# Kernel tuning notes

Hardware: AMD Instinct MI355X
Metric: run time of the kernel (lower is better)

The kernel has to match this reference:

```python
import jax, jax.numpy as jnp
import numpy as np

D_MODEL = 1024
H = 16
D_K = D_MODEL // H
B, S = 2, 2048


def setup_inputs() -> dict:
    key = jax.random.key(0)
    ks = jax.random.split(key, 11)
    sc = 1.0 / np.sqrt(D_MODEL)
    inp = {
        "q": jax.random.normal(ks[0], (B, S, D_MODEL), jnp.float32),
        "k": jax.random.normal(ks[1], (B, S, D_MODEL), jnp.float32),
        "v": jax.random.normal(ks[2], (B, S, D_MODEL), jnp.float32),
        "mask": jnp.ones((1, 1, S, S), dtype=bool),
        # nn.Linear weights are [out, in]; y = x @ W.T + b
        "wq_w": jax.random.normal(ks[3], (D_MODEL, D_MODEL), jnp.float32) * sc,
        "wq_b": jnp.zeros((D_MODEL,), jnp.float32),
        "wk_w": jax.random.normal(ks[4], (D_MODEL, D_MODEL), jnp.float32) * sc,
        "wk_b": jnp.zeros((D_MODEL,), jnp.float32),
        "wv_w": jax.random.normal(ks[5], (D_MODEL, D_MODEL), jnp.float32) * sc,
        "wv_b": jnp.zeros((D_MODEL,), jnp.float32),
        "wo_w": jax.random.normal(ks[6], (D_MODEL, D_MODEL), jnp.float32) * sc,
        "wo_b": jnp.zeros((D_MODEL,), jnp.float32),
    }
    return inp


def _split_heads(x):
    b, s, _ = x.shape
    return x.reshape(b, s, H, D_K).transpose(0, 2, 1, 3)  # [B,H,S,Dk]


def reference(q, k, v, mask, wq_w, wq_b, wk_w, wk_b, wv_w, wv_b, wo_w, wo_b):
    # projections (nn.Linear: x @ W.T + b)
    qh = _split_heads(q @ wq_w.T + wq_b)
    kh = _split_heads(k @ wk_w.T + wk_b)
    vh = _split_heads(v @ wv_w.T + wv_b)
    # scaled dot-product attention with additive -1e9 masking
    scores = jnp.einsum("bhqd,bhkd->bhqk", qh, kh) / jnp.sqrt(jnp.float32(D_K))
    scores = jnp.where(mask, scores, jnp.float32(-1e9))
    attn = jax.nn.softmax(scores, axis=-1)  # dropout p=0.0 -> identity
    out = jnp.einsum("bhqk,bhkd->bhqd", attn, vh)
    out = out.transpose(0, 2, 1, 3).reshape(q.shape[0], q.shape[1], D_MODEL)
    return out @ wo_w.T + wo_b
```

## Files before the change

kernel.cpp:

```cpp
#include <hip/hip_runtime.h>
#include <hip/hip_bf16.h>


typedef unsigned short u16;
typedef unsigned int u32;
typedef short s16x4 __attribute__((ext_vector_type(4)));
typedef short s16x8 __attribute__((ext_vector_type(8)));
typedef float f32x4 __attribute__((ext_vector_type(4)));
typedef unsigned int u32x2 __attribute__((ext_vector_type(2)));
typedef unsigned int u32x4 __attribute__((ext_vector_type(4)));

#define NH 16
#define SCQ 0.1803368801111204f

__device__ __forceinline__ float bf2f(u16 h) {
  u32 u = ((u32)h) << 16;
  return __builtin_bit_cast(float, u);
}
__device__ __forceinline__ u16 f2bf(float f) {
  u32 u = __builtin_bit_cast(u32, f);
  u32 r = (u + 0x7fffu + ((u >> 16) & 1u)) >> 16;
  return (u16)r;
}

__device__ __forceinline__ u32 pk2(float a, float b) {
#if __has_builtin(__builtin_amdgcn_cvt_pk_bf16_f32)
  typedef __bf16 bf2_t __attribute__((ext_vector_type(2)));
  bf2_t r = __builtin_amdgcn_cvt_pk_bf16_f32(a, b);
  return __builtin_bit_cast(u32, r);
#else
  u32 ua = __builtin_bit_cast(u32, a) + 0x8000u;
  u32 ub = __builtin_bit_cast(u32, b) + 0x8000u;
  return __builtin_amdgcn_perm(ub, ua, 0x07060302);
#endif
}

__device__ __forceinline__ void stage16(const void* g, void* l) {
  __builtin_amdgcn_global_load_lds((const __attribute__((address_space(1))) void*)g,
                                   (__attribute__((address_space(3))) void*)l,
                                   16, 0, 0);
}

#define BAR() __builtin_amdgcn_s_barrier()
#define WAITV2 asm volatile("s_waitcnt vmcnt(2)" ::: "memory")
#define WAITV0 asm volatile("s_waitcnt vmcnt(0)" ::: "memory")

__global__ __launch_bounds__(256) void convert_all(
    const float* __restrict__ q, const float* __restrict__ k,
    const float* __restrict__ v, const float* __restrict__ wq,
    const float* __restrict__ wk, const float* __restrict__ wv,
    const float* __restrict__ wo, u16* qb, u16* kb, u16* vb, u16* wqb,
    u16* wkb, u16* wvb, u16* wob) {
  const int y = blockIdx.y;
  const float* s;
  u16* d;
  int i;
  if (y < 3) {
    s = y == 0 ? q : (y == 1 ? k : v);
    d = y == 0 ? qb : (y == 1 ? kb : vb);
    i = (blockIdx.x * 256 + threadIdx.x) * 4;
  } else {
    int w = blockIdx.x >> 10, j = blockIdx.x & 1023;
    s = w == 0 ? wq : (w == 1 ? wk : (w == 2 ? wv : wo));
    d = w == 0 ? wqb : (w == 1 ? wkb : (w == 2 ? wvb : wob));
    i = (j * 256 + threadIdx.x) * 4;
  }
  f32x4 val = *(const f32x4*)(s + i);
  u32x2 o = {pk2(val[0], val[1]), pk2(val[2], val[3])};
  *(u32x2*)(d + i) = o;
}

#define GEMM_CORE(A_, W_)                                                      \
  const int tid = threadIdx.x;                                                 \
  const int lane = tid & 63;                                                   \
  const int wid = tid >> 6;                                                    \
  const int l16 = lane & 15, quad = lane >> 4;                                 \
  const int wm = (wid >> 1) * 64, wn = (wid & 1) * 64;                         \
  const int m0 = blockIdx.y * 128;                                             \
  const int n0 = blockIdx.x * 128;                                             \
  const int ra = tid >> 2;                                                     \
  const int c8 = (tid & 3) ^ (ra & 3);                                         \
  const u16* Abase = A_ + (size_t)(m0 + ra) * 1024 + c8 * 8;                   \
  const u16* A2 = Abase + (size_t)64 * 1024;                                   \
  const u16* Wbase = W_ + (size_t)(n0 + ra) * 1024 + c8 * 8;                   \
  const u16* W2 = Wbase + (size_t)64 * 1024;                                   \
  u16* ldsA = As + tid * 8;                                                    \
  u16* ldsB = Bs + tid * 8;                                                    \
  f32x4 acc[4][4];                                                             \
  _Pragma("unroll") for (int i = 0; i < 4; ++i)                                \
  _Pragma("unroll") for (int j = 0; j < 4; ++j)                                \
      acc[i][j] = (f32x4){0.f, 0.f, 0.f, 0.f};                                 \
  for (int k0 = 0; k0 < 1024; k0 += 32) {                                      \
    __syncthreads();                                                           \
    stage16(Abase + k0, ldsA);                                                 \
    stage16(A2 + k0, ldsA + 2048);                                             \
    stage16(Wbase + k0, ldsB);                                                 \
    stage16(W2 + k0, ldsB + 2048);                                             \
    __syncthreads();                                                           \
    s16x8 bfr[4];                                                              \
    _Pragma("unroll") for (int j = 0; j < 4; ++j) {                            \
      int row = wn + j * 16 + l16;                                             \
      bfr[j] = *(const s16x8*)&Bs[(row * 4 + (quad ^ (row & 3))) * 8];         \
    }                                                                          \
    _Pragma("unroll") for (int i = 0; i < 4; ++i) {                            \
      int row = wm + i * 16 + l16;                                             \
      s16x8 afr = *(const s16x8*)&As[(row * 4 + (quad ^ (row & 3))) * 8];      \
      _Pragma("unroll") for (int j = 0; j < 4; ++j)                            \
        acc[i][j] =                                                            \
            __builtin_amdgcn_mfma_f32_16x16x32_bf16(afr, bfr[j], acc[i][j],    \
                                                    0, 0, 0);                  \
    }                                                                          \
  }

__global__ __launch_bounds__(256, 3) void proj_kernel(
    const u16* __restrict__ q, const u16* __restrict__ k, const u16* __restrict__ v,
    const u16* __restrict__ wq, const u16* __restrict__ wk, const u16* __restrict__ wv,
    const float* __restrict__ bq, const float* __restrict__ bk,
    const float* __restrict__ bv,
    u16* __restrict__ Qh, u16* __restrict__ Kh, u16* __restrict__ VhT) {
  const int z = blockIdx.z;
  const u16* A_in = z == 0 ? q : (z == 1 ? k : v);
  const u16* W_in = z == 0 ? wq : (z == 1 ? wk : wv);
  const float* bias = z == 0 ? bq : (z == 1 ? bk : bv);

  __shared__ __align__(16) u16 As[128 * 32];
  __shared__ __align__(16) u16 Bs[128 * 32];

  GEMM_CORE(A_in, W_in)

  float bcol[4];
#pragma unroll
  for (int j = 0; j < 4; ++j) bcol[j] = bias[n0 + wn + j * 16 + l16];

  if (z < 2) {
    const float qs = (z == 0) ? SCQ : 1.0f;
    u16* out = (z == 0) ? Qh : Kh;
#pragma unroll
    for (int i = 0; i < 4; ++i) {
      int gm0 = m0 + wm + i * 16 + quad * 4;
      int b = gm0 >> 11, s = gm0 & 2047;
#pragma unroll
      for (int j = 0; j < 4; ++j) {
        int gn = n0 + wn + j * 16 + l16;
        int h = gn >> 6, dk = gn & 63;
        size_t base = ((size_t)(b * NH + h) * 2048 + s) * 64 + dk;
#pragma unroll
        for (int r = 0; r < 4; ++r)
          out[base + (size_t)r * 64] = f2bf((acc[i][j][r] + bcol[j]) * qs);
      }
    }
  } else {
#pragma unroll
    for (int i = 0; i < 4; ++i) {
      int gm0 = m0 + wm + i * 16 + quad * 4;
      int b = gm0 >> 11, s = gm0 & 2047;
#pragma unroll
      for (int j = 0; j < 4; ++j) {
        int gn = n0 + wn + j * 16 + l16;
        int h = gn >> 6, dk = gn & 63;
        size_t base = ((size_t)(b * NH + h) * 64 + dk) * 2048 + s;
        u32x2 pv = {pk2(acc[i][j][0] + bcol[j], acc[i][j][1] + bcol[j]),
                    pk2(acc[i][j][2] + bcol[j], acc[i][j][3] + bcol[j])};
        *(u32x2*)&VhT[base] = pv;
      }
    }
  }
}

__global__ __launch_bounds__(256, 3) void out_kernel(const u16* __restrict__ ctx,
                                                     const u16* __restrict__ wo,
                                                     const float* __restrict__ bo,
                                                     float* __restrict__ out) {
  __shared__ __align__(16) u16 As[128 * 32];
  __shared__ __align__(16) u16 Bs[128 * 32];

  GEMM_CORE(ctx, wo)

  float bcol[4];
#pragma unroll
  for (int j = 0; j < 4; ++j) bcol[j] = bo[n0 + wn + j * 16 + l16];

#pragma unroll
  for (int i = 0; i < 4; ++i) {
    int gm0 = m0 + wm + i * 16 + quad * 4;
#pragma unroll
    for (int j = 0; j < 4; ++j) {
      int gn = n0 + wn + j * 16 + l16;
#pragma unroll
      for (int r = 0; r < 4; ++r)
        out[(size_t)(gm0 + r) * 1024 + gn] = acc[i][j][r] + bcol[j];
    }
  }
}

__global__ __launch_bounds__(512, 4) void flash_kernel(const u16* __restrict__ Qh,
                                                       const u16* __restrict__ Kh,
                                                       const u16* __restrict__ VhT,
                                                       u16* __restrict__ ctx) {
  __shared__ __align__(16) u16 smem[16384];

  const int tid = threadIdx.x;
  const int lane = tid & 63;
  const int wid = tid >> 6;
  const int l16 = lane & 15, quad = lane >> 4;
  const int qt = blockIdx.x;
  const int bh = blockIdx.y;

  const u16* Qg = Qh + ((size_t)bh * 2048 + qt * 256) * 64;
  const u16* Kg = Kh + (size_t)bh * 2048 * 64;
  const u16* Vg = VhT + (size_t)bh * 64 * 2048;

  const int rq = tid >> 3;
  const int c8 = (tid & 7) ^ (rq & 7);
  const int gq = ((rq & 15) >> 2) * 8 + (rq & 3) + (((rq >> 4) & 1) << 2);
  const int ksrc = (rq & 32) + gq;

#define ISSUE_TILE(KT)                                                        \
  {                                                                           \
    stage16(Kg + (size_t)((KT) * 64 + ksrc) * 64 + c8 * 8,                    \
            smem + ((KT) & 1) * 4096 + tid * 8);                              \
    stage16(Vg + (size_t)rq * 2048 + (KT) * 64 + c8 * 8,                      \
            smem + 8192 + ((KT) & 1) * 4096 + tid * 8);                       \
  }

  u16* Qs = smem;
  s16x8 bq[2][2];
  for (int p = 0; p < 2; ++p) {
#pragma unroll
    for (int i = 0; i < 2; ++i)
      stage16(Qg + (size_t)(p * 128 + rq + i * 64) * 64 + c8 * 8,
              Qs + tid * 8 + i * 4096);
    __syncthreads();
    if ((wid >> 2) == p) {
#pragma unroll
      for (int ct = 0; ct < 2; ++ct) {
        int row = (wid & 3) * 32 + ct * 16 + l16;
#pragma unroll
        for (int kk = 0; kk < 2; ++kk)
          bq[ct][kk] =
              *(const s16x8*)&Qs[(row * 8 + ((kk * 4 + quad) ^ (row & 7))) * 8];
      }
    }
    asm volatile("s_waitcnt lgkmcnt(0)" ::: "memory");
    __syncthreads();
  }

  const s16x8 a1 = {0x3F80, 0x3F80, 0x3F80, 0x3F80,
                    0x3F80, 0x3F80, 0x3F80, 0x3F80};

  f32x4 lf[2];
  f32x4 oacc[4][2];
#pragma unroll
  for (int ct = 0; ct < 2; ++ct) lf[ct] = (f32x4){0.f, 0.f, 0.f, 0.f};
#pragma unroll
  for (int d = 0; d < 4; ++d)
#pragma unroll
    for (int ct = 0; ct < 2; ++ct) oacc[d][ct] = (f32x4){0.f, 0.f, 0.f, 0.f};

  ISSUE_TILE(0);

  for (int kt = 0; kt < 32; ++kt) {
    const u16* Ks = smem + (kt & 1) * 4096;
    const u16* Vs = smem + 8192 + (kt & 1) * 4096;

    BAR();
    if (kt < 31) {
      ISSUE_TILE(kt + 1);
      WAITV2;
    } else {
      WAITV0;
    }
    BAR();

    f32x4 st[4][2];
    __builtin_amdgcn_s_setprio(1);
#pragma unroll
    for (int rt = 0; rt < 4; ++rt) {
      int row = rt * 16 + l16;
      s16x8 ak0 = *(const s16x8*)&Ks[(row * 8 + (quad ^ (row & 7))) * 8];
      s16x8 ak1 = *(const s16x8*)&Ks[(row * 8 + ((4 + quad) ^ (row & 7))) * 8];
#pragma unroll
      for (int ct = 0; ct < 2; ++ct) {
        f32x4 t0 = __builtin_amdgcn_mfma_f32_16x16x32_bf16(
            ak0, bq[ct][0], (f32x4){0.f, 0.f, 0.f, 0.f}, 0, 0, 0);
        st[rt][ct] =
            __builtin_amdgcn_mfma_f32_16x16x32_bf16(ak1, bq[ct][1], t0, 0, 0, 0);
      }
    }
    __builtin_amdgcn_s_setprio(0);

#pragma unroll
    for (int rt = 0; rt < 4; ++rt)
#pragma unroll
      for (int ct = 0; ct < 2; ++ct)
#pragma unroll
        for (int c = 0; c < 4; ++c)
          st[rt][ct][c] = __builtin_exp2f(st[rt][ct][c]);

#pragma unroll
    for (int c = 0; c < 2; ++c) {
      s16x8 bp[2];
#pragma unroll
      for (int ct = 0; ct < 2; ++ct) {
        u32x4 bu = {pk2(st[2 * c][ct][0], st[2 * c][ct][1]),
                    pk2(st[2 * c][ct][2], st[2 * c][ct][3]),
                    pk2(st[2 * c + 1][ct][0], st[2 * c + 1][ct][1]),
                    pk2(st[2 * c + 1][ct][2], st[2 * c + 1][ct][3])};
        bp[ct] = __builtin_bit_cast(s16x8, bu);
      }
      __builtin_amdgcn_s_setprio(1);
#pragma unroll
      for (int ct = 0; ct < 2; ++ct)
        lf[ct] = __builtin_amdgcn_mfma_f32_16x16x32_bf16(a1, bp[ct], lf[ct],
                                                         0, 0, 0);
#pragma unroll
      for (int d = 0; d < 4; ++d) {
        int row = d * 16 + l16;
        s16x8 av = *(const s16x8*)&Vs[(row * 8 + ((c * 4 + quad) ^ (row & 7))) * 8];
#pragma unroll
        for (int ct = 0; ct < 2; ++ct)
          oacc[d][ct] = __builtin_amdgcn_mfma_f32_16x16x32_bf16(av, bp[ct],
                                                               oacc[d][ct], 0, 0, 0);
      }
      __builtin_amdgcn_s_setprio(0);
    }
  }

  const int bI = bh >> 4, hh = bh & 15;
#pragma unroll
  for (int ct = 0; ct < 2; ++ct) {
    int q = wid * 32 + ct * 16 + l16;
    float inv = 1.0f / lf[ct][0];
    size_t rowbase = ((size_t)bI * 2048 + qt * 256 + q) * 1024 + hh * 64;
#pragma unroll
    for (int d = 0; d < 4; ++d) {
      int dk0 = d * 16 + quad * 4;
      u32x2 pk = {pk2(oacc[d][ct][0] * inv, oacc[d][ct][1] * inv),
                  pk2(oacc[d][ct][2] * inv, oacc[d][ct][3] * inv)};
      *(u32x2*)&ctx[rowbase + dk0] = pk;
    }
  }
#undef ISSUE_TILE
}

extern "C" void kernel_launch(void* const* d_in, const int* in_sizes, int n_in,
                              void* d_out, int out_size, void* d_ws, size_t ws_size,
                              hipStream_t stream) {
  const float* q = (const float*)d_in[0];
  const float* k = (const float*)d_in[1];
  const float* v = (const float*)d_in[2];
  const float* wq = (const float*)d_in[4];
  const float* bq = (const float*)d_in[5];
  const float* wk = (const float*)d_in[6];
  const float* bk = (const float*)d_in[7];
  const float* wv = (const float*)d_in[8];
  const float* bv = (const float*)d_in[9];
  const float* wo = (const float*)d_in[10];
  const float* bo = (const float*)d_in[11];

  const size_t M1 = 1024 * 1024;
  u16* ws = (u16*)d_ws;
  u16* qb = ws;
  u16* kb = ws + 4 * M1;
  u16* vb = ws + 8 * M1;
  u16* wqb = ws + 12 * M1;
  u16* wkb = ws + 13 * M1;
  u16* wvb = ws + 14 * M1;
  u16* wob = ws + 15 * M1;
  u16* Qh = ws + 16 * M1;
  u16* Kh = ws + 20 * M1;
  u16* VhT = ws + 24 * M1;
  u16* ctx = kb;

  convert_all<<<dim3(4096, 4), 256, 0, stream>>>(q, k, v, wq, wk, wv, wo, qb, kb,
                                                 vb, wqb, wkb, wvb, wob);
  proj_kernel<<<dim3(8, 32, 3), 256, 0, stream>>>(qb, kb, vb, wqb, wkb, wvb,
                                                  bq, bk, bv, Qh, Kh, VhT);
  flash_kernel<<<dim3(8, 32), 512, 0, stream>>>(Qh, Kh, VhT, ctx);
  out_kernel<<<dim3(8, 32), 256, 0, stream>>>(ctx, wob, bo, (float*)d_out);
}
```

Measured before the change: 252.5 us.

## Fuse fp32-to-bf16 conversion into projection GEMM loads and drop convert kernel

Removes the separate conversion kernel and has the projection and output GEMMs load fp32 inputs and weights directly, converting to bf16 in registers before writing to LDS, with a register-prefetch of the next k-tile. This avoids one kernel launch and the write and re-read of bf16 copies of the activations and weights. The trade-off is that each GEMM tile now reads twice the bytes from global memory and repeats the conversion for every block that touches the same data. The flash kernel grid is also swapped so consecutive blocks cover different heads, which changes scheduling and cache locality.

```diff
diff --git a/kernel.cpp b/kernel.cpp
--- a/kernel.cpp
+++ b/kernel.cpp
@@ -13,10 +13,6 @@
 #define NH 16
 #define SCQ 0.1803368801111204f
 
-__device__ __forceinline__ float bf2f(u16 h) {
-  u32 u = ((u32)h) << 16;
-  return __builtin_bit_cast(float, u);
-}
 __device__ __forceinline__ u16 f2bf(float f) {
   u32 u = __builtin_bit_cast(u32, f);
   u32 r = (u + 0x7fffu + ((u >> 16) & 1u)) >> 16;
@@ -35,6 +31,11 @@
 #endif
 }
 
+__device__ __forceinline__ u32x4 pk8(f32x4 a, f32x4 b) {
+  return (u32x4){pk2(a[0], a[1]), pk2(a[2], a[3]), pk2(b[0], b[1]),
+                 pk2(b[2], b[3])};
+}
+
 __device__ __forceinline__ void stage16(const void* g, void* l) {
   __builtin_amdgcn_global_load_lds((const __attribute__((address_space(1))) void*)g,
                                    (__attribute__((address_space(3))) void*)l,
@@ -44,33 +45,9 @@
 #define BAR() __builtin_amdgcn_s_barrier()
 #define WAITV2 asm volatile("s_waitcnt vmcnt(2)" ::: "memory")
 #define WAITV0 asm volatile("s_waitcnt vmcnt(0)" ::: "memory")
-
-__global__ __launch_bounds__(256) void convert_all(
-    const float* __restrict__ q, const float* __restrict__ k,
-    const float* __restrict__ v, const float* __restrict__ wq,
-    const float* __restrict__ wk, const float* __restrict__ wv,
-    const float* __restrict__ wo, u16* qb, u16* kb, u16* vb, u16* wqb,
-    u16* wkb, u16* wvb, u16* wob) {
-  const int y = blockIdx.y;
-  const float* s;
-  u16* d;
-  int i;
-  if (y < 3) {
-    s = y == 0 ? q : (y == 1 ? k : v);
-    d = y == 0 ? qb : (y == 1 ? kb : vb);
-    i = (blockIdx.x * 256 + threadIdx.x) * 4;
-  } else {
-    int w = blockIdx.x >> 10, j = blockIdx.x & 1023;
-    s = w == 0 ? wq : (w == 1 ? wk : (w == 2 ? wv : wo));
-    d = w == 0 ? wqb : (w == 1 ? wkb : (w == 2 ? wvb : wob));
-    i = (j * 256 + threadIdx.x) * 4;
-  }
-  f32x4 val = *(const f32x4*)(s + i);
-  u32x2 o = {pk2(val[0], val[1]), pk2(val[2], val[3])};
-  *(u32x2*)(d + i) = o;
-}
-
-#define GEMM_CORE(A_, W_)                                                      \
+#define WAITLGKM asm volatile("s_waitcnt lgkmcnt(0)" ::: "memory")
+
+#define GEMM_IDX                                                               \
   const int tid = threadIdx.x;                                                 \
   const int lane = tid & 63;                                                   \
   const int wid = tid >> 6;                                                    \
@@ -80,23 +57,15 @@
   const int n0 = blockIdx.x * 128;                                             \
   const int ra = tid >> 2;                                                     \
   const int c8 = (tid & 3) ^ (ra & 3);                                         \
-  const u16* Abase = A_ + (size_t)(m0 + ra) * 1024 + c8 * 8;                   \
-  const u16* A2 = Abase + (size_t)64 * 1024;                                   \
-  const u16* Wbase = W_ + (size_t)(n0 + ra) * 1024 + c8 * 8;                   \
-  const u16* W2 = Wbase + (size_t)64 * 1024;                                   \
   u16* ldsA = As + tid * 8;                                                    \
   u16* ldsB = Bs + tid * 8;                                                    \
   f32x4 acc[4][4];                                                             \
   _Pragma("unroll") for (int i = 0; i < 4; ++i)                                \
   _Pragma("unroll") for (int j = 0; j < 4; ++j)                                \
-      acc[i][j] = (f32x4){0.f, 0.f, 0.f, 0.f};                                 \
-  for (int k0 = 0; k0 < 1024; k0 += 32) {                                      \
-    __syncthreads();                                                           \
-    stage16(Abase + k0, ldsA);                                                 \
-    stage16(A2 + k0, ldsA + 2048);                                             \
-    stage16(Wbase + k0, ldsB);                                                 \
-    stage16(W2 + k0, ldsB + 2048);                                             \
-    __syncthreads();                                                           \
+      acc[i][j] = (f32x4){0.f, 0.f, 0.f, 0.f};
+
+#define GEMM_COMPUTE                                                           \
+  {                                                                            \
     s16x8 bfr[4];                                                              \
     _Pragma("unroll") for (int j = 0; j < 4; ++j) {                            \
       int row = wn + j * 16 + l16;                                             \
@@ -113,20 +82,58 @@
   }
 
 __global__ __launch_bounds__(256, 3) void proj_kernel(
-    const u16* __restrict__ q, const u16* __restrict__ k, const u16* __restrict__ v,
-    const u16* __restrict__ wq, const u16* __restrict__ wk, const u16* __restrict__ wv,
+    const float* __restrict__ q, const float* __restrict__ k,
+    const float* __restrict__ v, const float* __restrict__ wq,
+    const float* __restrict__ wk, const float* __restrict__ wv,
     const float* __restrict__ bq, const float* __restrict__ bk,
     const float* __restrict__ bv,
     u16* __restrict__ Qh, u16* __restrict__ Kh, u16* __restrict__ VhT) {
   const int z = blockIdx.z;
-  const u16* A_in = z == 0 ? q : (z == 1 ? k : v);
-  const u16* W_in = z == 0 ? wq : (z == 1 ? wk : wv);
+  const float* A_in = z == 0 ? q : (z == 1 ? k : v);
+  const float* W_in = z == 0 ? wq : (z == 1 ? wk : wv);
   const float* bias = z == 0 ? bq : (z == 1 ? bk : bv);
 
   __shared__ __align__(16) u16 As[128 * 32];
   __shared__ __align__(16) u16 Bs[128 * 32];
 
-  GEMM_CORE(A_in, W_in)
+  GEMM_IDX
+
+  const float* Aof = A_in + (size_t)(m0 + ra) * 1024 + c8 * 8;
+  const float* A2of = Aof + (size_t)64 * 1024;
+  const float* Wof = W_in + (size_t)(n0 + ra) * 1024 + c8 * 8;
+  const float* W2of = Wof + (size_t)64 * 1024;
+
+  f32x4 rA[2], rA2[2], rW[2], rW2[2];
+  rA[0] = *(const f32x4*)(Aof);
+  rA[1] = *(const f32x4*)(Aof + 4);
+  rA2[0] = *(const f32x4*)(A2of);
+  rA2[1] = *(const f32x4*)(A2of + 4);
+  rW[0] = *(const f32x4*)(Wof);
+  rW[1] = *(const f32x4*)(Wof + 4);
+  rW2[0] = *(const f32x4*)(W2of);
+  rW2[1] = *(const f32x4*)(W2of + 4);
+
+  for (int k0 = 0; k0 < 1024; k0 += 32) {
+    BAR();
+    *(u32x4*)ldsA = pk8(rA[0], rA[1]);
+    *(u32x4*)(ldsA + 2048) = pk8(rA2[0], rA2[1]);
+    *(u32x4*)ldsB = pk8(rW[0], rW[1]);
+    *(u32x4*)(ldsB + 2048) = pk8(rW2[0], rW2[1]);
+    if (k0 < 992) {
+      const int kn = k0 + 32;
+      rA[0] = *(const f32x4*)(Aof + kn);
+      rA[1] = *(const f32x4*)(Aof + kn + 4);
+      rA2[0] = *(const f32x4*)(A2of + kn);
+      rA2[1] = *(const f32x4*)(A2of + kn + 4);
+      rW[0] = *(const f32x4*)(Wof + kn);
+      rW[1] = *(const f32x4*)(Wof + kn + 4);
+      rW2[0] = *(const f32x4*)(W2of + kn);
+      rW2[1] = *(const f32x4*)(W2of + kn + 4);
+    }
+    WAITLGKM;
+    BAR();
+    GEMM_COMPUTE
+  }
 
   float bcol[4];
 #pragma unroll
@@ -168,13 +175,41 @@
 }
 
 __global__ __launch_bounds__(256, 3) void out_kernel(const u16* __restrict__ ctx,
-                                                     const u16* __restrict__ wo,
+                                                     const float* __restrict__ wo,
                                                      const float* __restrict__ bo,
                                                      float* __restrict__ out) {
   __shared__ __align__(16) u16 As[128 * 32];
   __shared__ __align__(16) u16 Bs[128 * 32];
 
-  GEMM_CORE(ctx, wo)
+  GEMM_IDX
+
+  const u16* Abase = ctx + (size_t)(m0 + ra) * 1024 + c8 * 8;
+  const u16* A2 = Abase + (size_t)64 * 1024;
+  const float* Wof = wo + (size_t)(n0 + ra) * 1024 + c8 * 8;
+  const float* W2of = Wof + (size_t)64 * 1024;
+
+  f32x4 rW[2], rW2[2];
+  rW[0] = *(const f32x4*)(Wof);
+  rW[1] = *(const f32x4*)(Wof + 4);
+  rW2[0] = *(const f32x4*)(W2of);
+  rW2[1] = *(const f32x4*)(W2of + 4);
+
+  for (int k0 = 0; k0 < 1024; k0 += 32) {
+    __syncthreads();
+    stage16(Abase + k0, ldsA);
+    stage16(A2 + k0, ldsA + 2048);
+    *(u32x4*)ldsB = pk8(rW[0], rW[1]);
+    *(u32x4*)(ldsB + 2048) = pk8(rW2[0], rW2[1]);
+    if (k0 < 992) {
+      const int kn = k0 + 32;
+      rW[0] = *(const f32x4*)(Wof + kn);
+      rW[1] = *(const f32x4*)(Wof + kn + 4);
+      rW2[0] = *(const f32x4*)(W2of + kn);
+      rW2[1] = *(const f32x4*)(W2of + kn + 4);
+    }
+    __syncthreads();
+    GEMM_COMPUTE
+  }
 
   float bcol[4];
 #pragma unroll
@@ -203,8 +238,8 @@
   const int lane = tid & 63;
   const int wid = tid >> 6;
   const int l16 = lane & 15, quad = lane >> 4;
-  const int qt = blockIdx.x;
-  const int bh = blockIdx.y;
+  const int bh = blockIdx.x;
+  const int qt = blockIdx.y;
 
   const u16* Qg = Qh + ((size_t)bh * 2048 + qt * 256) * 64;
   const u16* Kg = Kh + (size_t)bh * 2048 * 64;
@@ -241,7 +276,7 @@
               *(const s16x8*)&Qs[(row * 8 + ((kk * 4 + quad) ^ (row & 7))) * 8];
       }
     }
-    asm volatile("s_waitcnt lgkmcnt(0)" ::: "memory");
+    WAITLGKM;
     __syncthreads();
   }
 
@@ -360,22 +395,13 @@
 
   const size_t M1 = 1024 * 1024;
   u16* ws = (u16*)d_ws;
-  u16* qb = ws;
-  u16* kb = ws + 4 * M1;
-  u16* vb = ws + 8 * M1;
-  u16* wqb = ws + 12 * M1;
-  u16* wkb = ws + 13 * M1;
-  u16* wvb = ws + 14 * M1;
-  u16* wob = ws + 15 * M1;
-  u16* Qh = ws + 16 * M1;
-  u16* Kh = ws + 20 * M1;
-  u16* VhT = ws + 24 * M1;
-  u16* ctx = kb;
-
-  convert_all<<<dim3(4096, 4), 256, 0, stream>>>(q, k, v, wq, wk, wv, wo, qb, kb,
-                                                 vb, wqb, wkb, wvb, wob);
-  proj_kernel<<<dim3(8, 32, 3), 256, 0, stream>>>(qb, kb, vb, wqb, wkb, wvb,
+  u16* Qh = ws;
+  u16* Kh = ws + 4 * M1;
+  u16* VhT = ws + 8 * M1;
+  u16* ctx = ws + 12 * M1;
+
+  proj_kernel<<<dim3(8, 32, 3), 256, 0, stream>>>(q, k, v, wq, wk, wv,
                                                   bq, bk, bv, Qh, Kh, VhT);
-  flash_kernel<<<dim3(8, 32), 512, 0, stream>>>(Qh, Kh, VhT, ctx);
-  out_kernel<<<dim3(8, 32), 256, 0, stream>>>(ctx, wob, bo, (float*)d_out);
-}
+  flash_kernel<<<dim3(32, 8), 512, 0, stream>>>(Qh, Kh, VhT, ctx);
+  out_kernel<<<dim3(8, 32), 256, 0, stream>>>(ctx, wo, bo, (float*)d_out);
+}
```

Result: slower. 279.6 us (+10.7%).
